# Optimization experiments

Measured on AMD Instinct MI355X. Metric: run time of the kernel, lower is better.

The kernel has to match this reference:

```python
import jax, jax.numpy as jnp
import numpy as np

T, H, N = 4096, 32, 64  # seq_length, num_heads, head_size


def setup_inputs() -> dict:
    key = jax.random.key(0)
    ks = jax.random.split(key, 7)
    shape = (T, H * N)
    r = jax.random.normal(ks[0], shape, jnp.float32)
    # w is a per-channel time-decay in (0, 1)
    w = jax.random.uniform(ks[1], shape, jnp.float32, minval=0.1, maxval=0.999)
    k = jax.random.normal(ks[2], shape, jnp.float32) * 0.3
    v = jax.random.normal(ks[3], shape, jnp.float32) * 0.3
    # a (in-context removal) and b (replacement key) kept small for numerical stability of the 4096-step scan
    a = jax.random.normal(ks[4], shape, jnp.float32) * 0.1
    b = jax.random.normal(ks[5], shape, jnp.float32) * 0.1
    state2 = jax.random.normal(ks[6], (H, N, N), jnp.float32) * 0.1
    return {"seq_length": T, "r": r, "w": w, "k": k, "v": v, "a": a, "b": b, "state2": state2}


def reference(seq_length, r, w, k, v, a, b, state2):
    # reshape flat [T, H*N] inputs to per-head vectors [T, H, N]
    rh = r.reshape(seq_length, H, N)
    wh = w.reshape(seq_length, H, N)
    kh = k.reshape(seq_length, H, N)
    vh = v.reshape(seq_length, H, N)
    ah = a.reshape(seq_length, H, N)
    bh = b.reshape(seq_length, H, N)

    def step(s, xs):
        r_t, w_t, k_t, v_t, a_t, b_t = xs  # each [H, N]
        # state @ a : [H,N,N] x [H,N,1] -> [H,N]
        sa = jnp.einsum('hij,hj->hi', s, a_t)
        # s*w (column-wise decay) + (s@a)@b (rank-1) + v k^T (rank-1)
        s = s * w_t[:, None, :] + sa[:, :, None] * b_t[:, None, :] + v_t[:, :, None] * k_t[:, None, :]
        # x_t = state @ r : [H, N]
        x_t = jnp.einsum('hij,hj->hi', s, r_t)
        return s, x_t

    state2_out, xs = jax.lax.scan(step, state2, (rh, wh, kh, vh, ah, bh))
    x = xs.reshape(seq_length, H, 1, N)
    return x, state2_out
```

## Files before the change

kernel.cpp:

```cpp
#include <hip/hip_runtime.h>


static constexpr int T_LEN = 4096;
static constexpr int H_HEADS = 32;
static constexpr int N_DIM = 64;
static constexpr int HN = H_HEADS * N_DIM;
static constexpr int WPB = 8;
static constexpr int BT = WPB * 64;
static constexpr int NB = (H_HEADS * N_DIM) / WPB;
static constexpr int C = 16;
static constexpr int TC = T_LEN / C;

typedef int int32x4_t __attribute__((ext_vector_type(4)));
__device__ float llvm_amdgcn_raw_buffer_load_fp32(int32x4_t srsrc, int voffset,
                                                  int soffset, int glc_slc)
    __asm("llvm.amdgcn.raw.buffer.load.f32");

__device__ __forceinline__ int32x4_t make_srd(const void* p, unsigned bytes) {
  int32x4_t r;
  r.x = (int)(unsigned long long)p;
  r.y = (int)((unsigned long long)p >> 32);
  r.z = (int)bytes;
  r.w = 0x00020000;
  return r;
}

__device__ __forceinline__ float wave_sum_bcast(float x) {
  asm volatile(
      "s_nop 1\n\t"
      "v_add_f32 %0, %0, %0 row_shr:1 bound_ctrl:0\n\t"
      "s_nop 1\n\t"
      "v_add_f32 %0, %0, %0 row_shr:2 bound_ctrl:0\n\t"
      "s_nop 1\n\t"
      "v_add_f32 %0, %0, %0 row_shr:4 bound_ctrl:0\n\t"
      "s_nop 1\n\t"
      "v_add_f32 %0, %0, %0 row_shr:8 bound_ctrl:0\n\t"
      "s_nop 1\n\t"
      "v_add_f32 %0, %0, %0 row_bcast:15 row_mask:0xa\n\t"
      "s_nop 1\n\t"
      "v_add_f32 %0, %0, %0 row_bcast:31 row_mask:0xc\n\t"
      "s_nop 1\n\t"
      : "+v"(x));
  return __int_as_float(__builtin_amdgcn_readlane(__float_as_int(x), 63));
}

__device__ __forceinline__ void wave_sum2(float& x, float& y) {
  asm volatile(
      "s_nop 1\n\t"
      "v_add_f32 %0, %0, %0 row_shr:1 bound_ctrl:0\n\t"
      "v_add_f32 %1, %1, %1 row_shr:1 bound_ctrl:0\n\t"
      "s_nop 0\n\t"
      "v_add_f32 %0, %0, %0 row_shr:2 bound_ctrl:0\n\t"
      "v_add_f32 %1, %1, %1 row_shr:2 bound_ctrl:0\n\t"
      "s_nop 0\n\t"
      "v_add_f32 %0, %0, %0 row_shr:4 bound_ctrl:0\n\t"
      "v_add_f32 %1, %1, %1 row_shr:4 bound_ctrl:0\n\t"
      "s_nop 0\n\t"
      "v_add_f32 %0, %0, %0 row_shr:8 bound_ctrl:0\n\t"
      "v_add_f32 %1, %1, %1 row_shr:8 bound_ctrl:0\n\t"
      "s_nop 0\n\t"
      "v_add_f32 %0, %0, %0 row_bcast:15 row_mask:0xa\n\t"
      "v_add_f32 %1, %1, %1 row_bcast:15 row_mask:0xa\n\t"
      "s_nop 0\n\t"
      "v_add_f32 %0, %0, %0 row_bcast:31 row_mask:0xc\n\t"
      "v_add_f32 %1, %1, %1 row_bcast:31 row_mask:0xc\n\t"
      "s_nop 1\n\t"
      : "+v"(x), "+v"(y));
}

__global__ __launch_bounds__(BT, 2) void wkv7_scan(
    const float* __restrict__ rp, const float* __restrict__ wp,
    const float* __restrict__ kp, const float* __restrict__ vp,
    const float* __restrict__ ap, const float* __restrict__ bp,
    const float* __restrict__ s0p, float* __restrict__ xp,
    float* __restrict__ sop) {
  const int tid  = threadIdx.x;
  const int lane = tid & 63;
  const int wv   = tid >> 6;
  const int blk  = blockIdx.x;
  const int h     = blk & (H_HEADS - 1);
  const int ibase = (blk >> 5) * WPB;
  const int i     = ibase + wv;
  const int hb    = h * N_DIM;

  __shared__ float sw[2][C][N_DIM], sA[2][C][N_DIM], sB[2][C][N_DIM],
                   sK[2][C][N_DIM], sR[2][C][N_DIM];
  __shared__ float sV[2][C][WPB];
  __shared__ float xbuf[WPB][65];

  constexpr unsigned ARR_BYTES = (unsigned)T_LEN * HN * 4u;
  const int32x4_t srd_r = make_srd(rp, ARR_BYTES);
  const int32x4_t srd_w = make_srd(wp, ARR_BYTES);
  const int32x4_t srd_k = make_srd(kp, ARR_BYTES);
  const int32x4_t srd_v = make_srd(vp, ARR_BYTES);
  const int32x4_t srd_a = make_srd(ap, ARR_BYTES);
  const int32x4_t srd_b = make_srd(bp, ARR_BYTES);

  float s = s0p[(size_t)(hb + i) * N_DIM + lane];

  const int j   = lane;
  const int u0  = tid >> 6;
  const int vo0 = (u0 * HN + j) << 2;
  const int vo1 = vo0 + (8 * HN << 2);
  const int sbase = hb << 2;
  const int uv  = tid >> 3;
  const int qv  = tid & 7;
  const int vov = (uv * HN + qv) << 2;
  const int svbase = (hb + ibase) << 2;

  float g0, g1, g2, g3, g4, g5, g6, g7, g8, g9, g10;

#define STAGE_LOAD(CI)                                                   \
  do {                                                                   \
    const int so = (CI) * (C * HN * 4) + sbase;                          \
    g0 = llvm_amdgcn_raw_buffer_load_fp32(srd_w, vo0, so, 0);            \
    g1 = llvm_amdgcn_raw_buffer_load_fp32(srd_a, vo0, so, 0);            \
    g2 = llvm_amdgcn_raw_buffer_load_fp32(srd_b, vo0, so, 0);            \
    g3 = llvm_amdgcn_raw_buffer_load_fp32(srd_k, vo0, so, 0);            \
    g4 = llvm_amdgcn_raw_buffer_load_fp32(srd_r, vo0, so, 0);            \
    g5 = llvm_amdgcn_raw_buffer_load_fp32(srd_w, vo1, so, 0);            \
    g6 = llvm_amdgcn_raw_buffer_load_fp32(srd_a, vo1, so, 0);            \
    g7 = llvm_amdgcn_raw_buffer_load_fp32(srd_b, vo1, so, 0);            \
    g8 = llvm_amdgcn_raw_buffer_load_fp32(srd_k, vo1, so, 0);            \
    g9 = llvm_amdgcn_raw_buffer_load_fp32(srd_r, vo1, so, 0);            \
    if (wv < 2)                                                          \
      g10 = llvm_amdgcn_raw_buffer_load_fp32(                            \
          srd_v, vov, (CI) * (C * HN * 4) + svbase, 0);                  \
  } while (0)

#define STAGE_STORE(BI)                                                  \
  do {                                                                   \
    sw[BI][u0][j] = g0;  sA[BI][u0][j] = g1;  sB[BI][u0][j] = g2;        \
    sK[BI][u0][j] = g3;  sR[BI][u0][j] = g4;                             \
    sw[BI][u0 + 8][j] = g5;  sA[BI][u0 + 8][j] = g6;                     \
    sB[BI][u0 + 8][j] = g7;  sK[BI][u0 + 8][j] = g8;                     \
    sR[BI][u0 + 8][j] = g9;                                              \
    if (wv < 2) sV[BI][uv][qv] = g10;                                    \
  } while (0)

  float xacc = 0.0f;

  STAGE_LOAD(0);
  STAGE_STORE(0);
  __syncthreads();

  float sa;
  {
    float p0 = s * sA[0][0][lane];
    sa = wave_sum_bcast(p0);
  }

  for (int c = 0; c < TC; ++c) {
    const int bi = c & 1;

    STAGE_LOAD(c + 1);
    __builtin_amdgcn_sched_barrier(0);

    float lw = sw[bi][0][lane], lb = sB[bi][0][lane], lk = sK[bi][0][lane],
          lr = sR[bi][0][lane], lv = sV[bi][0][wv];
    float la1 = sA[bi][1][lane];
    float lr15 = 0.0f;
#pragma unroll
    for (int u = 0; u < C; ++u) {
      const int un = (u < C - 1) ? u + 1 : u;
      const float nw = sw[bi][un][lane], nb = sB[bi][un][lane],
                  nk = sK[bi][un][lane], nr = sR[bi][un][lane],
                  nv = sV[bi][un][wv];
      const float na = (u < C - 2) ? sA[bi][u + 2][lane] : 0.0f;

      s = fmaf(s, lw, fmaf(sa, lb, lv * lk));

      if (u < C - 1) {
        float px = s * lr, pa = s * la1;
        wave_sum2(px, pa);
        const float xv =
            __int_as_float(__builtin_amdgcn_readlane(__float_as_int(px), 63));
        sa = __int_as_float(__builtin_amdgcn_readlane(__float_as_int(pa), 63));
        const int tl = ((c & 3) << 4) | u;
        xacc = (lane == tl) ? xv : xacc;
      } else {
        lr15 = lr;
      }

      lw = nw; lb = nb; lk = nk; lr = nr; lv = nv; la1 = na;
    }

    __builtin_amdgcn_sched_barrier(0);
    STAGE_STORE(bi ^ 1);
    __syncthreads();

    {
      float la0 = sA[bi ^ 1][0][lane];
      float px = s * lr15, pa = s * la0;
      wave_sum2(px, pa);
      const float xv =
          __int_as_float(__builtin_amdgcn_readlane(__float_as_int(px), 63));
      sa = __int_as_float(__builtin_amdgcn_readlane(__float_as_int(pa), 63));
      const int tl = ((c & 3) << 4) | 15;
      xacc = (lane == tl) ? xv : xacc;
    }

    if ((c & 3) == 3) {
      xbuf[wv][lane] = xacc;
      __syncthreads();
      const int tl2 = tid >> 3;
      const int iw  = tid & 7;
      const int t0  = (c + 1) * C - 64;
      xp[(size_t)(t0 + tl2) * HN + hb + ibase + iw] = xbuf[iw][tl2];
    }
  }

#undef STAGE_LOAD
#undef STAGE_STORE

  sop[(size_t)(hb + i) * N_DIM + lane] = s;
}

extern "C" void kernel_launch(void* const* d_in, const int* in_sizes, int n_in,
                              void* d_out, int out_size, void* d_ws, size_t ws_size,
                              hipStream_t stream) {
  const float* r  = (const float*)d_in[1];
  const float* w  = (const float*)d_in[2];
  const float* k  = (const float*)d_in[3];
  const float* v  = (const float*)d_in[4];
  const float* a  = (const float*)d_in[5];
  const float* b  = (const float*)d_in[6];
  const float* s0 = (const float*)d_in[7];
  float* x    = (float*)d_out;
  float* sout = x + (size_t)T_LEN * H_HEADS * N_DIM;

  wkv7_scan<<<dim3(NB), dim3(BT), 0, stream>>>(r, w, k, v, a, b, s0, x, sout);
}
```

Baseline: 678.8 us.

## Precompute per-step dot products to take reductions off the serial scan path

Adds a pre-pass kernel that computes the per-timestep, per-head scalars b·a_{t+1}, k·a_{t+1}, b·r and k·r into workspace. The scan then computes s·(w⊙a) and s·(w⊙r) from the old state in parallel with the state update, and forms x_t and the next sa by scalar FMAs. This breaks the dependency where each step's reduction had to wait for the freshly updated state, shortening the serial critical path. The cost is an extra kernel launch, extra global traffic for the scalars, and a different floating-point summation order.

Result: slower. 815.5 us (+20.1%).

```diff
diff --git a/kernel.cpp b/kernel.cpp
--- a/kernel.cpp
+++ b/kernel.cpp
@@ -68,12 +68,50 @@
       : "+v"(x), "+v"(y));
 }
 
+__global__ __launch_bounds__(256) void wkv7_pre(
+    const float* __restrict__ rp, const float* __restrict__ kp,
+    const float* __restrict__ ap, const float* __restrict__ bp,
+    float* __restrict__ scw) {
+  const int tid  = threadIdx.x;
+  const int lane = tid & 63;
+  const int wv   = tid >> 6;
+  const int wid  = blockIdx.x * 4 + wv;
+  const int t    = wid >> 5;
+  const int h    = wid & 31;
+  const int hb   = h * N_DIM;
+
+  constexpr unsigned ARR_BYTES = (unsigned)T_LEN * HN * 4u;
+  const int32x4_t srd_r = make_srd(rp, ARR_BYTES);
+  const int32x4_t srd_k = make_srd(kp, ARR_BYTES);
+  const int32x4_t srd_a = make_srd(ap, ARR_BYTES);
+  const int32x4_t srd_b = make_srd(bp, ARR_BYTES);
+
+  const int vo    = lane << 2;
+  const int so_t  = (t * HN + hb) << 2;
+  const int so_t1 = ((t + 1) * HN + hb) << 2;
+
+  const float bv = llvm_amdgcn_raw_buffer_load_fp32(srd_b, vo, so_t, 0);
+  const float kv = llvm_amdgcn_raw_buffer_load_fp32(srd_k, vo, so_t, 0);
+  const float rv = llvm_amdgcn_raw_buffer_load_fp32(srd_r, vo, so_t, 0);
+  const float a1 = llvm_amdgcn_raw_buffer_load_fp32(srd_a, vo, so_t1, 0);
+
+  float pba = bv * a1, pka = kv * a1;
+  float pbr = bv * rv, pkr = kv * rv;
+  wave_sum2(pba, pka);
+  wave_sum2(pbr, pkr);
+  if (lane == 63) {
+    float4 o;
+    o.x = pba; o.y = pka; o.z = pbr; o.w = pkr;
+    *(float4*)(scw + ((size_t)h * T_LEN + t) * 4) = o;
+  }
+}
+
 __global__ __launch_bounds__(BT, 2) void wkv7_scan(
     const float* __restrict__ rp, const float* __restrict__ wp,
     const float* __restrict__ kp, const float* __restrict__ vp,
     const float* __restrict__ ap, const float* __restrict__ bp,
     const float* __restrict__ s0p, float* __restrict__ xp,
-    float* __restrict__ sop) {
+    float* __restrict__ sop, const float* __restrict__ scp) {
   const int tid  = threadIdx.x;
   const int lane = tid & 63;
   const int wv   = tid >> 6;
@@ -86,17 +124,21 @@
   __shared__ float sw[2][C][N_DIM], sA[2][C][N_DIM], sB[2][C][N_DIM],
                    sK[2][C][N_DIM], sR[2][C][N_DIM];
   __shared__ float sV[2][C][WPB];
+  __shared__ __align__(16) float sSC[2][C * 4];
   __shared__ float xbuf[WPB][65];
 
   constexpr unsigned ARR_BYTES = (unsigned)T_LEN * HN * 4u;
+  constexpr unsigned SC_BYTES  = (unsigned)T_LEN * H_HEADS * 4u * 4u;
   const int32x4_t srd_r = make_srd(rp, ARR_BYTES);
   const int32x4_t srd_w = make_srd(wp, ARR_BYTES);
   const int32x4_t srd_k = make_srd(kp, ARR_BYTES);
   const int32x4_t srd_v = make_srd(vp, ARR_BYTES);
   const int32x4_t srd_a = make_srd(ap, ARR_BYTES);
   const int32x4_t srd_b = make_srd(bp, ARR_BYTES);
+  const int32x4_t srd_c = make_srd(scp, SC_BYTES);
 
   float s = s0p[(size_t)(hb + i) * N_DIM + lane];
+  const float a0v = ap[hb + lane];
 
   const int j   = lane;
   const int u0  = tid >> 6;
@@ -107,25 +149,30 @@
   const int qv  = tid & 7;
   const int vov = (uv * HN + qv) << 2;
   const int svbase = (hb + ibase) << 2;
-
-  float g0, g1, g2, g3, g4, g5, g6, g7, g8, g9, g10;
+  const int voc = lane << 2;
+  const int scbase = h * (T_LEN * 16);
+
+  float g0, g1, g2, g3, g4, g5, g6, g7, g8, g9, g10, g11;
 
 #define STAGE_LOAD(CI)                                                   \
   do {                                                                   \
     const int so = (CI) * (C * HN * 4) + sbase;                          \
     g0 = llvm_amdgcn_raw_buffer_load_fp32(srd_w, vo0, so, 0);            \
-    g1 = llvm_amdgcn_raw_buffer_load_fp32(srd_a, vo0, so, 0);            \
+    g1 = llvm_amdgcn_raw_buffer_load_fp32(srd_a, vo0, so + (HN << 2), 0);\
     g2 = llvm_amdgcn_raw_buffer_load_fp32(srd_b, vo0, so, 0);            \
     g3 = llvm_amdgcn_raw_buffer_load_fp32(srd_k, vo0, so, 0);            \
     g4 = llvm_amdgcn_raw_buffer_load_fp32(srd_r, vo0, so, 0);            \
     g5 = llvm_amdgcn_raw_buffer_load_fp32(srd_w, vo1, so, 0);            \
-    g6 = llvm_amdgcn_raw_buffer_load_fp32(srd_a, vo1, so, 0);            \
+    g6 = llvm_amdgcn_raw_buffer_load_fp32(srd_a, vo1, so + (HN << 2), 0);\
     g7 = llvm_amdgcn_raw_buffer_load_fp32(srd_b, vo1, so, 0);            \
     g8 = llvm_amdgcn_raw_buffer_load_fp32(srd_k, vo1, so, 0);            \
     g9 = llvm_amdgcn_raw_buffer_load_fp32(srd_r, vo1, so, 0);            \
     if (wv < 2)                                                          \
       g10 = llvm_amdgcn_raw_buffer_load_fp32(                            \
           srd_v, vov, (CI) * (C * HN * 4) + svbase, 0);                  \
+    if (wv == 2)                                                         \
+      g11 = llvm_amdgcn_raw_buffer_load_fp32(                            \
+          srd_c, voc, (CI) * (C * 16) + scbase, 0);                      \
   } while (0)
 
 #define STAGE_STORE(BI)                                                  \
@@ -136,19 +183,19 @@
     sB[BI][u0 + 8][j] = g7;  sK[BI][u0 + 8][j] = g8;                     \
     sR[BI][u0 + 8][j] = g9;                                              \
     if (wv < 2) sV[BI][uv][qv] = g10;                                    \
+    if (wv == 2) sSC[BI][lane] = g11;                                    \
   } while (0)
 
   float xacc = 0.0f;
 
   STAGE_LOAD(0);
   STAGE_STORE(0);
-  __syncthreads();
-
   float sa;
   {
-    float p0 = s * sA[0][0][lane];
+    float p0 = s * a0v;
     sa = wave_sum_bcast(p0);
   }
+  __syncthreads();
 
   for (int c = 0; c < TC; ++c) {
     const int bi = c & 1;
@@ -156,49 +203,41 @@
     STAGE_LOAD(c + 1);
     __builtin_amdgcn_sched_barrier(0);
 
-    float lw = sw[bi][0][lane], lb = sB[bi][0][lane], lk = sK[bi][0][lane],
-          lr = sR[bi][0][lane], lv = sV[bi][0][wv];
-    float la1 = sA[bi][1][lane];
-    float lr15 = 0.0f;
+    float lw = sw[bi][0][lane], la = sA[bi][0][lane], lb = sB[bi][0][lane],
+          lk = sK[bi][0][lane], lr = sR[bi][0][lane], lv = sV[bi][0][wv];
+    float4 scv = *(const float4*)&sSC[bi][0];
 #pragma unroll
     for (int u = 0; u < C; ++u) {
       const int un = (u < C - 1) ? u + 1 : u;
-      const float nw = sw[bi][un][lane], nb = sB[bi][un][lane],
-                  nk = sK[bi][un][lane], nr = sR[bi][un][lane],
-                  nv = sV[bi][un][wv];
-      const float na = (u < C - 2) ? sA[bi][u + 2][lane] : 0.0f;
+      const float nw = sw[bi][un][lane], na = sA[bi][un][lane],
+                  nb = sB[bi][un][lane], nk = sK[bi][un][lane],
+                  nr = sR[bi][un][lane], nv = sV[bi][un][wv];
+      const float4 nscv = *(const float4*)&sSC[bi][un * 4];
+
+      const float wa = lw * la;
+      const float wr = lw * lr;
+      float pq = s * wa;
+      float px = s * wr;
+      wave_sum2(pq, px);
+      const float Qa =
+          __int_as_float(__builtin_amdgcn_readlane(__float_as_int(pq), 63));
+      const float Qr =
+          __int_as_float(__builtin_amdgcn_readlane(__float_as_int(px), 63));
 
       s = fmaf(s, lw, fmaf(sa, lb, lv * lk));
 
-      if (u < C - 1) {
-        float px = s * lr, pa = s * la1;
-        wave_sum2(px, pa);
-        const float xv =
-            __int_as_float(__builtin_amdgcn_readlane(__float_as_int(px), 63));
-        sa = __int_as_float(__builtin_amdgcn_readlane(__float_as_int(pa), 63));
-        const int tl = ((c & 3) << 4) | u;
-        xacc = (lane == tl) ? xv : xacc;
-      } else {
-        lr15 = lr;
-      }
-
-      lw = nw; lb = nb; lk = nk; lr = nr; lv = nv; la1 = na;
+      const float xv = fmaf(sa, scv.z, fmaf(lv, scv.w, Qr));
+      sa             = fmaf(sa, scv.x, fmaf(lv, scv.y, Qa));
+
+      const int tl = ((c & 3) << 4) | u;
+      xacc = (lane == tl) ? xv : xacc;
+
+      lw = nw; la = na; lb = nb; lk = nk; lr = nr; lv = nv; scv = nscv;
     }
 
     __builtin_amdgcn_sched_barrier(0);
     STAGE_STORE(bi ^ 1);
     __syncthreads();
-
-    {
-      float la0 = sA[bi ^ 1][0][lane];
-      float px = s * lr15, pa = s * la0;
-      wave_sum2(px, pa);
-      const float xv =
-          __int_as_float(__builtin_amdgcn_readlane(__float_as_int(px), 63));
-      sa = __int_as_float(__builtin_amdgcn_readlane(__float_as_int(pa), 63));
-      const int tl = ((c & 3) << 4) | 15;
-      xacc = (lane == tl) ? xv : xacc;
-    }
 
     if ((c & 3) == 3) {
       xbuf[wv][lane] = xacc;
@@ -228,6 +267,8 @@
   const float* s0 = (const float*)d_in[7];
   float* x    = (float*)d_out;
   float* sout = x + (size_t)T_LEN * H_HEADS * N_DIM;
-
-  wkv7_scan<<<dim3(NB), dim3(BT), 0, stream>>>(r, w, k, v, a, b, s0, x, sout);
-}
+  float* scw  = (float*)d_ws;
+
+  wkv7_pre<<<dim3(T_LEN * H_HEADS / 4), dim3(256), 0, stream>>>(r, k, a, b, scw);
+  wkv7_scan<<<dim3(NB), dim3(BT), 0, stream>>>(r, w, k, v, a, b, s0, x, sout, scw);
+}
```
